# Performance work log

Hardware: AMD Instinct MI355X
Metric: run time of the kernel (lower is better)

## Reference

```python
import jax, jax.numpy as jnp
import numpy as np


def setup_inputs() -> dict:
    key = jax.random.key(0)
    k1, k2, k3 = jax.random.split(key, 3)
    L, B, D = 2048, 32, 512  # seq_len, batch, input_size == hidden_size == output_size
    NUM_MATRICES = 3  # has_skip_term and input_size == output_size
    x = jax.random.normal(k1, (L, B, D), dtype=jnp.float32)
    # transform_module: Linear(D, D * 3, bias=False), xavier_uniform-like scale
    W = jax.random.normal(k2, (D, D * NUM_MATRICES), dtype=jnp.float32) * (1.0 / np.sqrt(D))
    # weight_c ~ U(-weight_c_init, weight_c_init), shape (2*D,)
    weight_c = jax.random.uniform(k3, (2 * D,), dtype=jnp.float32, minval=-1.0, maxval=1.0)
    # bias: zeros; highway_bias (=0.0) added to second half -> all zeros
    bias = jnp.zeros((2 * D,), dtype=jnp.float32)
    return {"x": x, "W": W, "weight_c": weight_c, "bias": bias}


def reference(x, W, weight_c, bias):
    # x: (L, B, D); W: (D, 3D); weight_c, bias: (2D,)
    L, B, D = x.shape
    # U = transform_module(x): batched matmul, then view as (L, B, D, 3)
    U = jnp.einsum('lbi,io->lbo', x, W).reshape(L, B, D, 3)
    wc_f, wc_r = weight_c[:D], weight_c[D:]  # forget / reset peephole weights
    b_f, b_r = bias[:D], bias[D:]            # forget / reset (highway) biases

    def step(c_prev, inp):
        u, res = inp  # u: (B, D, 3); res: (B, D) residual (= x_t, skip term)
        fg = jax.nn.sigmoid(u[..., 1] + wc_f * c_prev + b_f)
        rg = jax.nn.sigmoid(u[..., 2] + wc_r * c_prev + b_r)
        c = fg * c_prev + (1.0 - fg) * u[..., 0]
        # activation_type == 0 -> g(c) = c; scale_val is None (rescale=False)
        h = rg * c + (1.0 - rg) * res
        return c, h

    c0 = jnp.zeros((B, D), dtype=x.dtype)
    c_last, h = jax.lax.scan(step, c0, (U, x))
    return h, c_last
```

## Files before the change

### kernel.cpp

```cpp
#include <hip/hip_runtime.h>

#define LL 2048
#define BB 32
#define DD 512
#define NN (3 * DD)
#define KK (DD)

#define SCH 16
#define NCH (LL / SCH)
#define TP 20

typedef short bf16x8 __attribute__((ext_vector_type(8)));
typedef float f32x4 __attribute__((ext_vector_type(4)));

__device__ __forceinline__ unsigned short f2bf(float f) {
  unsigned u = __builtin_bit_cast(unsigned, f);
  u += 0x7fffu + ((u >> 16) & 1u);
  return (unsigned short)(u >> 16);
}

__global__ __launch_bounds__(256) void cvt_w_kernel(const float* __restrict__ W,
                                                    unsigned short* __restrict__ Wt) {
  int j = blockIdx.x * 256 + threadIdx.x;
  int i  = j & (KK - 1);
  int op = j >> 9;
  int g  = op >> 9;
  int dd = op & (DD - 1);
  Wt[j] = f2bf(W[(size_t)i * NN + dd * 3 + g]);
}

__global__ __launch_bounds__(256, 2) void fused_kernel(
    const float* __restrict__ x, const unsigned short* __restrict__ Wt,
    const float* __restrict__ wc, const float* __restrict__ bias,
    float* __restrict__ out) {
  __shared__ __align__(16) unsigned short xbuf[2][SCH * DD];
  __shared__ __align__(16) float ubt[2][3][32][TP];
  __shared__ __align__(16) float rbuf[4][SCH][32];

  const int n   = blockIdx.x;
  const int xcd = n & 7;
  const int idx = n >> 3;
  const int b   = xcd * 4 + (idx >> 4);
  const int d0  = (idx & 15) << 5;

  const int wv   = threadIdx.x >> 6;
  const int lane = threadIdx.x & 63;

  if (wv < 3) {
    const int quad = lane >> 4;
    const int l16  = lane & 15;
    bf16x8 wf0[16], wf1[16];
    {
      const unsigned short* wp0 = Wt + (size_t)(wv * DD + d0 + l16) * KK + quad * 8;
      const unsigned short* wp1 = wp0 + (size_t)16 * KK;
#pragma unroll
      for (int j = 0; j < 16; ++j) {
        wf0[j] = *(const bf16x8*)(wp0 + j * 32);
        wf1[j] = *(const bf16x8*)(wp1 + j * 32);
      }
    }
    const int gl    = wv * 64 + lane;
    const int abase = l16 * 1024;
    const int aswz  = (l16 & 7) << 4;
    const int c16lo = d0 >> 3;

    for (int s = 0; s <= NCH + 1; ++s) {
      float4 sa[6], sb[6];
      const bool do_stage = (s < NCH);
      const bool t6 = (gl < 64);
      if (do_stage) {
#pragma unroll
        for (int i = 0; i < 5; ++i) {
          int bid = gl + 192 * i;
          int row = bid >> 6, c16 = bid & 63;
          const float* sp = x + ((size_t)(s * SCH + row) * BB + b) * DD + c16 * 8;
          sa[i] = *(const float4*)sp; sb[i] = *(const float4*)(sp + 4);
        }
        if (t6) {
          int bid = 960 + gl;
          int row = bid >> 6, c16 = bid & 63;
          const float* sp = x + ((size_t)(s * SCH + row) * BB + b) * DD + c16 * 8;
          sa[5] = *(const float4*)sp; sb[5] = *(const float4*)(sp + 4);
        }
      }
      if (s >= 1 && s <= NCH) {
        const char* xb = (const char*)xbuf[(s - 1) & 1];
        f32x4 acc0 = {}, acc1 = {};
#pragma unroll
        for (int j = 0; j < 16; ++j) {
          bf16x8 af = *(const bf16x8*)(xb + abase + ((j * 64 + quad * 16) ^ aswz));
          acc0 = __builtin_amdgcn_mfma_f32_16x16x32_bf16(af, wf0[j], acc0, 0, 0, 0);
          acc1 = __builtin_amdgcn_mfma_f32_16x16x32_bf16(af, wf1[j], acc1, 0, 0, 0);
        }
        float* ug = &ubt[(s - 1) & 1][wv][0][0];
        *(f32x4*)&ug[l16 * TP + quad * 4]        = acc0;
        *(f32x4*)&ug[(16 + l16) * TP + quad * 4] = acc1;
      }
      if (do_stage) {
        char*  xw = (char*)xbuf[s & 1];
        float* rw = &rbuf[s & 3][0][0];
#pragma unroll
        for (int i = 0; i < 5; ++i) {
          int bid = gl + 192 * i;
          int row = bid >> 6, c16 = bid & 63;
          int cg = c16 - c16lo;
          if ((unsigned)cg < 4u) {
            *(float4*)&rw[row * 32 + cg * 8]     = sa[i];
            *(float4*)&rw[row * 32 + cg * 8 + 4] = sb[i];
          }
          union { bf16x8 v; unsigned short u[8]; } o;
          o.u[0]=f2bf(sa[i].x); o.u[1]=f2bf(sa[i].y); o.u[2]=f2bf(sa[i].z); o.u[3]=f2bf(sa[i].w);
          o.u[4]=f2bf(sb[i].x); o.u[5]=f2bf(sb[i].y); o.u[6]=f2bf(sb[i].z); o.u[7]=f2bf(sb[i].w);
          *(bf16x8*)(xw + row * 1024 + ((c16 * 16) ^ ((row & 7) << 4))) = o.v;
        }
        if (t6) {
          int bid = 960 + gl;
          int row = bid >> 6, c16 = bid & 63;
          int cg = c16 - c16lo;
          if ((unsigned)cg < 4u) {
            *(float4*)&rw[row * 32 + cg * 8]     = sa[5];
            *(float4*)&rw[row * 32 + cg * 8 + 4] = sb[5];
          }
          union { bf16x8 v; unsigned short u[8]; } o;
          o.u[0]=f2bf(sa[5].x); o.u[1]=f2bf(sa[5].y); o.u[2]=f2bf(sa[5].z); o.u[3]=f2bf(sa[5].w);
          o.u[4]=f2bf(sb[5].x); o.u[5]=f2bf(sb[5].y); o.u[6]=f2bf(sb[5].z); o.u[7]=f2bf(sb[5].w);
          *(bf16x8*)(xw + row * 1024 + ((c16 * 16) ^ ((row & 7) << 4))) = o.v;
        }
      }
      __syncthreads();
    }
  } else {
    const int ch = lane;
    const float kln = 1.442695040888963f;
    float pf0 = 0.f, pr0 = 0.f, pf1 = 0.f, pr1 = 0.f, c = 0.f;
    float* hp = nullptr;
    if (ch < 32) {
      const int d = d0 + ch;
      float wcf = wc[d], wcr = wc[DD + d];
      pf0 = -kln * bias[d];      pr0 = -kln * bias[DD + d];
      pf1 = -kln * wcf;          pr1 = -kln * wcr;
      hp = out + (size_t)b * DD + d;
    }
    for (int s = 0; s <= NCH + 1; ++s) {
      if (s >= 2 && ch < 32) {
        const int cc = s - 2;
        const float* ub = &ubt[cc & 1][0][0][0];
        const float* rb = &rbuf[cc & 3][0][0];
        float u0v[SCH], u1v[SCH], u2v[SCH], xrv[SCH];
#pragma unroll
        for (int j = 0; j < 4; ++j) {
          float4 q0 = *(const float4*)&ub[        ch * TP + j * 4];
          float4 q1 = *(const float4*)&ub[ 640 +  ch * TP + j * 4];
          float4 q2 = *(const float4*)&ub[1280 +  ch * TP + j * 4];
          u0v[j*4+0]=q0.x; u0v[j*4+1]=q0.y; u0v[j*4+2]=q0.z; u0v[j*4+3]=q0.w;
          u1v[j*4+0]=q1.x; u1v[j*4+1]=q1.y; u1v[j*4+2]=q1.z; u1v[j*4+3]=q1.w;
          u2v[j*4+0]=q2.x; u2v[j*4+1]=q2.y; u2v[j*4+2]=q2.z; u2v[j*4+3]=q2.w;
        }
#pragma unroll
        for (int t = 0; t < SCH; ++t) xrv[t] = rb[t * 32 + ch];
#pragma unroll
        for (int t = 0; t < SCH; ++t) {
          float tf = __builtin_fmaf(pf1, c, __builtin_fmaf(-kln, u1v[t], pf0));
          float tr = __builtin_fmaf(pr1, c, __builtin_fmaf(-kln, u2v[t], pr0));
          float fg = __builtin_amdgcn_rcpf(1.0f + __builtin_amdgcn_exp2f(tf));
          float rg = __builtin_amdgcn_rcpf(1.0f + __builtin_amdgcn_exp2f(tr));
          c = __builtin_fmaf(fg, c - u0v[t], u0v[t]);
          *hp = __builtin_fmaf(rg, c - xrv[t], xrv[t]);
          hp += BB * DD;
        }
      }
      __syncthreads();
    }
    if (ch < 32)
      out[(size_t)LL * BB * DD + (size_t)b * DD + d0 + ch] = c;
  }
}

extern "C" void kernel_launch(void* const* d_in, const int* in_sizes, int n_in,
                              void* d_out, int out_size, void* d_ws, size_t ws_size,
                              hipStream_t stream) {
  const float* x    = (const float*)d_in[0];
  const float* W    = (const float*)d_in[1];
  const float* wc   = (const float*)d_in[2];
  const float* bias = (const float*)d_in[3];
  float* out = (float*)d_out;

  unsigned short* Wt = (unsigned short*)d_ws;

  cvt_w_kernel<<<(NN * KK) / 256, 256, 0, stream>>>(W, Wt);
  fused_kernel<<<BB * (DD / 32), 256, 0, stream>>>(x, Wt, wc, bias, out);
}
```

Before: 412.1 us.

## Prefetch next x chunk across barrier and tile-transpose weight conversion

The producer waves now load the next chunk of x into registers one full iteration ahead, so the global load latency spans the MFMA work and the barrier instead of being exposed within one iteration. The stored registers are written to shared memory at the start of the following iteration. Separately, the weight bf16 conversion kernel now transposes through a padded shared tile, so both the global reads and the global writes are coalesced. Keeping the prefetched registers live across the loop raises register pressure in the producer waves.

After: 383.2 us. 1.08x faster.

```diff
diff --git a/kernel.cpp b/kernel.cpp
--- a/kernel.cpp
+++ b/kernel.cpp
@@ -21,12 +21,26 @@
 
 __global__ __launch_bounds__(256) void cvt_w_kernel(const float* __restrict__ W,
                                                     unsigned short* __restrict__ Wt) {
-  int j = blockIdx.x * 256 + threadIdx.x;
-  int i  = j & (KK - 1);
-  int op = j >> 9;
-  int g  = op >> 9;
-  int dd = op & (DD - 1);
-  Wt[j] = f2bf(W[(size_t)i * NN + dd * 3 + g]);
+  __shared__ float tile[64][65];
+  const int k0  = (blockIdx.x & 7) * 64;
+  const int o0  = (blockIdx.x >> 3) * 64;
+  const int tid = threadIdx.x;
+#pragma unroll
+  for (int i = 0; i < 16; ++i) {
+    int flat = i * 256 + tid;
+    int kk = flat >> 6, oo = flat & 63;
+    tile[kk][oo] = W[(size_t)(k0 + kk) * NN + o0 + oo];
+  }
+  __syncthreads();
+#pragma unroll
+  for (int i = 0; i < 16; ++i) {
+    int flat = i * 256 + tid;
+    int oo = flat >> 6, kk = flat & 63;
+    int o  = o0 + oo;
+    int g  = o - 3 * (o / 3);
+    int dd = o / 3;
+    Wt[(size_t)(g * DD + dd) * KK + k0 + kk] = f2bf(tile[kk][oo]);
+  }
 }
 
 __global__ __launch_bounds__(256, 2) void fused_kernel(
@@ -63,26 +77,61 @@
     const int abase = l16 * 1024;
     const int aswz  = (l16 & 7) << 4;
     const int c16lo = d0 >> 3;
-
+    const bool t6   = (gl < 64);
+
+    float4 sa[6], sb[6];
+
+#define ISSUE(ch)                                                            \
+    do {                                                                     \
+      _Pragma("unroll") for (int i = 0; i < 5; ++i) {                        \
+        int bid = gl + 192 * i;                                              \
+        int row = bid >> 6, c16 = bid & 63;                                  \
+        const float* sp = x + ((size_t)((ch) * SCH + row) * BB + b) * DD + c16 * 8; \
+        sa[i] = *(const float4*)sp; sb[i] = *(const float4*)(sp + 4);        \
+      }                                                                      \
+      if (t6) {                                                              \
+        int bid = 960 + gl; int row = bid >> 6, c16 = bid & 63;              \
+        const float* sp = x + ((size_t)((ch) * SCH + row) * BB + b) * DD + c16 * 8; \
+        sa[5] = *(const float4*)sp; sb[5] = *(const float4*)(sp + 4);        \
+      }                                                                      \
+    } while (0)
+
+#define WRITE(ch)                                                            \
+    do {                                                                     \
+      char*  xw = (char*)xbuf[(ch) & 1];                                     \
+      float* rw = &rbuf[(ch) & 3][0][0];                                     \
+      _Pragma("unroll") for (int i = 0; i < 5; ++i) {                        \
+        int bid = gl + 192 * i;                                              \
+        int row = bid >> 6, c16 = bid & 63;                                  \
+        int cg = c16 - c16lo;                                                \
+        if ((unsigned)cg < 4u) {                                             \
+          *(float4*)&rw[row * 32 + cg * 8]     = sa[i];                      \
+          *(float4*)&rw[row * 32 + cg * 8 + 4] = sb[i];                      \
+        }                                                                    \
+        union { bf16x8 v; unsigned short u[8]; } o;                          \
+        o.u[0]=f2bf(sa[i].x); o.u[1]=f2bf(sa[i].y); o.u[2]=f2bf(sa[i].z); o.u[3]=f2bf(sa[i].w); \
+        o.u[4]=f2bf(sb[i].x); o.u[5]=f2bf(sb[i].y); o.u[6]=f2bf(sb[i].z); o.u[7]=f2bf(sb[i].w); \
+        *(bf16x8*)(xw + row * 1024 + ((c16 * 16) ^ ((row & 7) << 4))) = o.v; \
+      }                                                                      \
+      if (t6) {                                                              \
+        int bid = 960 + gl;                                                  \
+        int row = bid >> 6, c16 = bid & 63;                                  \
+        int cg = c16 - c16lo;                                                \
+        if ((unsigned)cg < 4u) {                                             \
+          *(float4*)&rw[row * 32 + cg * 8]     = sa[5];                      \
+          *(float4*)&rw[row * 32 + cg * 8 + 4] = sb[5];                      \
+        }                                                                    \
+        union { bf16x8 v; unsigned short u[8]; } o;                          \
+        o.u[0]=f2bf(sa[5].x); o.u[1]=f2bf(sa[5].y); o.u[2]=f2bf(sa[5].z); o.u[3]=f2bf(sa[5].w); \
+        o.u[4]=f2bf(sb[5].x); o.u[5]=f2bf(sb[5].y); o.u[6]=f2bf(sb[5].z); o.u[7]=f2bf(sb[5].w); \
+        *(bf16x8*)(xw + row * 1024 + ((c16 * 16) ^ ((row & 7) << 4))) = o.v; \
+      }                                                                      \
+    } while (0)
+
+    ISSUE(0);
     for (int s = 0; s <= NCH + 1; ++s) {
-      float4 sa[6], sb[6];
-      const bool do_stage = (s < NCH);
-      const bool t6 = (gl < 64);
-      if (do_stage) {
-#pragma unroll
-        for (int i = 0; i < 5; ++i) {
-          int bid = gl + 192 * i;
-          int row = bid >> 6, c16 = bid & 63;
-          const float* sp = x + ((size_t)(s * SCH + row) * BB + b) * DD + c16 * 8;
-          sa[i] = *(const float4*)sp; sb[i] = *(const float4*)(sp + 4);
-        }
-        if (t6) {
-          int bid = 960 + gl;
-          int row = bid >> 6, c16 = bid & 63;
-          const float* sp = x + ((size_t)(s * SCH + row) * BB + b) * DD + c16 * 8;
-          sa[5] = *(const float4*)sp; sb[5] = *(const float4*)(sp + 4);
-        }
-      }
+      if (s < NCH) WRITE(s);
+      if (s + 1 < NCH) ISSUE(s + 1);
       if (s >= 1 && s <= NCH) {
         const char* xb = (const char*)xbuf[(s - 1) & 1];
         f32x4 acc0 = {}, acc1 = {};
@@ -96,39 +145,10 @@
         *(f32x4*)&ug[l16 * TP + quad * 4]        = acc0;
         *(f32x4*)&ug[(16 + l16) * TP + quad * 4] = acc1;
       }
-      if (do_stage) {
-        char*  xw = (char*)xbuf[s & 1];
-        float* rw = &rbuf[s & 3][0][0];
-#pragma unroll
-        for (int i = 0; i < 5; ++i) {
-          int bid = gl + 192 * i;
-          int row = bid >> 6, c16 = bid & 63;
-          int cg = c16 - c16lo;
-          if ((unsigned)cg < 4u) {
-            *(float4*)&rw[row * 32 + cg * 8]     = sa[i];
-            *(float4*)&rw[row * 32 + cg * 8 + 4] = sb[i];
-          }
-          union { bf16x8 v; unsigned short u[8]; } o;
-          o.u[0]=f2bf(sa[i].x); o.u[1]=f2bf(sa[i].y); o.u[2]=f2bf(sa[i].z); o.u[3]=f2bf(sa[i].w);
-          o.u[4]=f2bf(sb[i].x); o.u[5]=f2bf(sb[i].y); o.u[6]=f2bf(sb[i].z); o.u[7]=f2bf(sb[i].w);
-          *(bf16x8*)(xw + row * 1024 + ((c16 * 16) ^ ((row & 7) << 4))) = o.v;
-        }
-        if (t6) {
-          int bid = 960 + gl;
-          int row = bid >> 6, c16 = bid & 63;
-          int cg = c16 - c16lo;
-          if ((unsigned)cg < 4u) {
-            *(float4*)&rw[row * 32 + cg * 8]     = sa[5];
-            *(float4*)&rw[row * 32 + cg * 8 + 4] = sb[5];
-          }
-          union { bf16x8 v; unsigned short u[8]; } o;
-          o.u[0]=f2bf(sa[5].x); o.u[1]=f2bf(sa[5].y); o.u[2]=f2bf(sa[5].z); o.u[3]=f2bf(sa[5].w);
-          o.u[4]=f2bf(sb[5].x); o.u[5]=f2bf(sb[5].y); o.u[6]=f2bf(sb[5].z); o.u[7]=f2bf(sb[5].w);
-          *(bf16x8*)(xw + row * 1024 + ((c16 * 16) ^ ((row & 7) << 4))) = o.v;
-        }
-      }
       __syncthreads();
     }
+#undef ISSUE
+#undef WRITE
   } else {
     const int ch = lane;
     const float kln = 1.442695040888963f;
@@ -187,6 +207,6 @@
 
   unsigned short* Wt = (unsigned short*)d_ws;
 
-  cvt_w_kernel<<<(NN * KK) / 256, 256, 0, stream>>>(W, Wt);
+  cvt_w_kernel<<<8 * 24, 256, 0, stream>>>(W, Wt);
   fused_kernel<<<BB * (DD / 32), 256, 0, stream>>>(x, Wt, wc, bias, out);
 }
```
